# Kernel optimization log

Measured on AMD Instinct MI355X. Metric: run time of the kernel, lower is better.

## Reference

```python
import jax, jax.numpy as jnp
import numpy as np

N = 30000   # nodes
E = 480000  # directed edges (avg degree 16)
CIN = 64    # c_in
CH = 64     # c_hidden

_PARAM_NAMES = ["Wl1","bl1","Wr1","br1","We1","att1","bo1",
                "Wlm","blm","Wrm","brm","Wem","attm","bom",
                "Wl8","bl8","Wr8","br8","We8","att8","bo8"]
_PARAM_SHAPES = [(CIN,CH),(CH,),(CIN,CH),(CH,),(1,CH),(CH,),(CH,),
                 (6,CH,CH),(6,CH),(6,CH,CH),(6,CH),(6,1,CH),(6,CH),(6,CH),
                 (CH,1),(1,),(CH,1),(1,),(1,1),(1,),(1,)]

def setup_inputs() -> dict:
    key = jax.random.key(0)
    ks = jax.random.split(key, 4 + len(_PARAM_NAMES))
    inp = {
        "features": jax.random.normal(ks[0], (N, CIN), dtype=jnp.float32),
        "edge_src": jax.random.randint(ks[1], (E,), 0, N),
        "edge_dst": jax.random.randint(ks[2], (E,), 0, N),
        "edge_weight": jax.random.uniform(ks[3], (E,), dtype=jnp.float32),
    }
    for i, (name, shape) in enumerate(zip(_PARAM_NAMES, _PARAM_SHAPES)):
        inp[name] = jax.random.normal(ks[4 + i], shape, dtype=jnp.float32) * 0.05
    return inp

def _gatv2_layer(x, src, dst, attr, Wl, bl, Wr, br, We, att, bo):
    # PyG GATv2Conv, heads=1, negative_slope=0.2; (src,dst,attr) already include self-loops.
    n = x.shape[0]
    xl = x @ Wl + bl                                  # [N, C] source-side transform (lin_l)
    xr = x @ Wr + br                                  # [N, C] target-side transform (lin_r)
    e = xl[src] + xr[dst] + attr[:, None] * We[0]     # [Ea, C] per-edge pre-activation
    logit = jax.nn.leaky_relu(e, 0.2) @ att           # [Ea]
    m = jax.ops.segment_max(logit, dst, num_segments=n)
    z = jnp.exp(logit - m[dst])                       # stable softmax over each node's in-edges
    s = jax.ops.segment_sum(z, dst, num_segments=n)
    alpha = z / s[dst]                                # [Ea]
    return jax.ops.segment_sum(alpha[:, None] * xl[src], dst, num_segments=n) + bo

def reference(features, edge_src, edge_dst, edge_weight,
              Wl1, bl1, Wr1, br1, We1, att1, bo1,
              Wlm, blm, Wrm, brm, Wem, attm, bom,
              Wl8, bl8, Wr8, br8, We8, att8, bo8):
    n = features.shape[0]
    # add_self_loops=True with fill_value='mean': self-loop attr = mean of incoming edge attrs
    cnt = jax.ops.segment_sum(jnp.ones_like(edge_weight), edge_dst, num_segments=n)
    loop_attr = jax.ops.segment_sum(edge_weight, edge_dst, num_segments=n) / jnp.maximum(cnt, 1.0)
    loops = jnp.arange(n)
    src = jnp.concatenate([edge_src, loops])
    dst = jnp.concatenate([edge_dst, loops])
    attr = jnp.concatenate([edge_weight, loop_attr])
    x = _gatv2_layer(features, src, dst, attr, Wl1, bl1, Wr1, br1, We1, att1, bo1)
    for i in range(6):  # conv2..conv7, structurally identical hidden layers
        x = _gatv2_layer(x, src, dst, attr, Wlm[i], blm[i], Wrm[i], brm[i], Wem[i], attm[i], bom[i])
    x = _gatv2_layer(x, src, dst, attr, Wl8, bl8, Wr8, br8, We8, att8, bo8)  # [N, 1]
    return jnp.mean(x, axis=-2)  # mean pool over nodes -> [1]
```

## Files before the change

kernel.cpp:

```cpp
#include <hip/hip_runtime.h>
#include <math.h>

#define CH 64

__device__ __forceinline__ void multi_reduce8(const float lv[8], float L[8], int lane) {
  bool b5 = (lane & 32) != 0;
  float r1[4];
#pragma unroll
  for (int j = 0; j < 4; ++j) {
    float keep = b5 ? lv[j + 4] : lv[j];
    float send = b5 ? lv[j] : lv[j + 4];
    r1[j] = keep + __shfl_xor(send, 32, 64);
  }
  bool b4 = (lane & 16) != 0;
  float r2[2];
#pragma unroll
  for (int j = 0; j < 2; ++j) {
    float keep = b4 ? r1[j + 2] : r1[j];
    float send = b4 ? r1[j] : r1[j + 2];
    r2[j] = keep + __shfl_xor(send, 16, 64);
  }
  bool b3 = (lane & 8) != 0;
  float keep = b3 ? r2[1] : r2[0];
  float send = b3 ? r2[0] : r2[1];
  float v = keep + __shfl_xor(send, 8, 64);
  v += __shfl_xor(v, 4, 64);
  v += __shfl_xor(v, 2, 64);
  v += __shfl_xor(v, 1, 64);
#pragma unroll
  for (int j = 0; j < 8; ++j) L[j] = __shfl(v, j * 8, 64);
}


#define WSUM_SCALE 33554432.0f
#define WSUM_MASK 0xFFFFFFFFFFULL

__global__ void k_count(const int* __restrict__ dst, const float* __restrict__ w, int E,
                        unsigned long long* __restrict__ agg, int* __restrict__ rank) {
  int i = blockIdx.x * blockDim.x + threadIdx.x;
  if (i < E) {
    int d = dst[i];
    unsigned long long pk =
        (1ULL << 40) | (unsigned long long)(w[i] * WSUM_SCALE);
    unsigned long long old = atomicAdd(&agg[d], pk);
    rank[i] = (int)(old >> 40);
  }
}

__global__ void k_alloc(const unsigned long long* __restrict__ agg,
                        float* __restrict__ loop_attr, int* __restrict__ deg,
                        int* __restrict__ row_beg, int* __restrict__ total, int n) {
  int i = blockIdx.x * blockDim.x + threadIdx.x;
  int lane = threadIdx.x & 63;
  int d = 0;
  if (i < n) {
    unsigned long long v = agg[i];
    int c = (int)(v >> 40);
    float ws = (float)(v & WSUM_MASK) * (1.0f / WSUM_SCALE);
    loop_attr[i] = ws / fmaxf((float)c, 1.0f);
    d = c + 1;
    deg[i] = d;
  }
  int x = d;
#pragma unroll
  for (int off = 1; off < 64; off <<= 1) {
    int t = __shfl_up(x, off, 64);
    if (lane >= off) x += t;
  }
  int base = 0;
  if (lane == 63) base = atomicAdd(total, x);
  base = __shfl(base, 63, 64);
  if (i < n) row_beg[i] = base + x - d;
}

__global__ void k_scatter(const int* __restrict__ src, const int* __restrict__ dst,
                          const float* __restrict__ w, const int* __restrict__ rank, int E,
                          const int* __restrict__ row_beg, int2* __restrict__ csr) {
  int i = blockIdx.x * blockDim.x + threadIdx.x;
  if (i < E) {
    int d = dst[i];
    csr[row_beg[d] + rank[i]] = make_int2(src[i], __float_as_int(w[i]));
  }
}

__global__ void k_selfloop(int n, const int* __restrict__ row_beg, const int* __restrict__ deg,
                           int2* __restrict__ csr, const float* __restrict__ loop_attr) {
  int v = blockIdx.x * blockDim.x + threadIdx.x;
  if (v < n) {
    csr[row_beg[v] + deg[v] - 1] = make_int2(v, __float_as_int(loop_attr[v]));
  }
}


__global__ void __launch_bounds__(256) k_transform(
    const float* __restrict__ x, const float* __restrict__ Wl, const float* __restrict__ bl,
    const float* __restrict__ Wr, const float* __restrict__ br,
    float* __restrict__ xl, float* __restrict__ xr, int n) {
  __shared__ float sW[2][CH * CH];
  for (int i = threadIdx.x; i < (CH * CH) / 4; i += blockDim.x) {
    ((float4*)sW[0])[i] = ((const float4*)Wl)[i];
    ((float4*)sW[1])[i] = ((const float4*)Wr)[i];
  }
  __syncthreads();
  int lane = threadIdx.x & 63;
  int wid = threadIdx.x >> 6;
  float blc = bl[lane], brc = br[lane];
  int wavesPerGrid = (gridDim.x * blockDim.x) >> 6;
  for (int row = blockIdx.x * (blockDim.x >> 6) + wid; row < n; row += wavesPerGrid) {
    float xv = x[(size_t)row * CH + lane];
    float accl = blc, accr = brc;
#pragma unroll
    for (int k = 0; k < CH; ++k) {
      float xk = __shfl(xv, k, 64);
      accl = fmaf(xk, sW[0][k * CH + lane], accl);
      accr = fmaf(xk, sW[1][k * CH + lane], accr);
    }
    xl[(size_t)row * CH + lane] = accl;
    xr[(size_t)row * CH + lane] = accr;
  }
}


__global__ void __launch_bounds__(256) k_aggregate(
    const float* __restrict__ xl, const float* __restrict__ xr,
    const int* __restrict__ row_beg, const int* __restrict__ deg,
    const int2* __restrict__ csr,
    const float* __restrict__ We, const float* __restrict__ att, const float* __restrict__ bo,
    float* __restrict__ out, int n) {
  int lane = threadIdx.x & 63;
  int v = (blockIdx.x * blockDim.x + threadIdx.x) >> 6;
  if (v >= n) return;
  float Wec = We[lane], attc = att[lane], boc = bo[lane];
  float xrc = xr[(size_t)v * CH + lane];
  int beg = row_beg[v], dv = deg[v];
  float m = -INFINITY, s = 0.f, acc = 0.f;
  for (int chunk = 0; chunk < dv; chunk += 64) {
    int nc = min(64, dv - chunk);
    int2 ed = (lane < nc) ? csr[beg + chunk + lane] : make_int2(0, 0);
    for (int e = 0; e < nc; e += 8) {
      float xv[8], lv[8], L[8];
#pragma unroll
      for (int j = 0; j < 8; ++j) {
        int sj = __shfl(ed.x, e + j, 64);
        xv[j] = xl[(size_t)sj * CH + lane];
      }
#pragma unroll
      for (int j = 0; j < 8; ++j) {
        float aj = __int_as_float(__shfl(ed.y, e + j, 64));
        float ee = fmaf(aj, Wec, xv[j] + xrc);
        lv[j] = (ee > 0.f ? ee : 0.2f * ee) * attc;
      }
      multi_reduce8(lv, L, lane);
#pragma unroll
      for (int j = 0; j < 8; ++j)
        if (e + j >= nc) L[j] = -INFINITY;
      float bm = fmaxf(fmaxf(fmaxf(L[0], L[1]), fmaxf(L[2], L[3])),
                       fmaxf(fmaxf(L[4], L[5]), fmaxf(L[6], L[7])));
      float mn = fmaxf(m, bm);
      float sc = __expf(m - mn);
      float psum = 0.f, pdot = 0.f;
#pragma unroll
      for (int j = 0; j < 8; ++j) {
        float p = __expf(L[j] - mn);
        psum += p;
        pdot = fmaf(p, xv[j], pdot);
      }
      s = fmaf(s, sc, psum);
      acc = fmaf(acc, sc, pdot);
      m = mn;
    }
  }
  out[(size_t)v * CH + lane] = acc / s + boc;
}

__global__ void __launch_bounds__(256) k_transform8(
    const float* __restrict__ x, const float* __restrict__ Wl, const float* __restrict__ bl,
    const float* __restrict__ Wr, const float* __restrict__ br,
    float* __restrict__ xl8, float* __restrict__ xr8, int n) {
  int lane = threadIdx.x & 63;
  int v = (blockIdx.x * blockDim.x + threadIdx.x) >> 6;
  if (v >= n) return;
  float xv = x[(size_t)v * CH + lane];
  float a = xv * Wl[lane];
  float b = xv * Wr[lane];
#pragma unroll
  for (int off = 32; off > 0; off >>= 1) {
    a += __shfl_xor(a, off, 64);
    b += __shfl_xor(b, off, 64);
  }
  if (lane == 0) {
    xl8[v] = a + bl[0];
    xr8[v] = b + br[0];
  }
}

__global__ void __launch_bounds__(256) k_agg8_mean(
    const float* __restrict__ xl8, const float* __restrict__ xr8,
    const int* __restrict__ row_beg, const int* __restrict__ deg,
    const int2* __restrict__ csr,
    const float* __restrict__ We, const float* __restrict__ att, const float* __restrict__ bo,
    float* __restrict__ out, int n) {
  int lane = threadIdx.x & 63;
  int wid = threadIdx.x >> 6;
  float We0 = We[0], att0 = att[0], bo0 = bo[0];
  float inv_n = 1.0f / (float)n;
  float local = 0.f;
  int nwaves = gridDim.x * 4;
  for (int v = blockIdx.x * 4 + wid; v < n; v += nwaves) {
    float xrc = xr8[v];
    int beg = row_beg[v], dv = deg[v];
    float m = -INFINITY, s = 0.f, acc = 0.f;
    for (int chunk = 0; chunk < dv; chunk += 64) {
      int idx = chunk + lane;
      bool valid = idx < dv;
      int2 ed = valid ? csr[beg + idx] : make_int2(0, 0);
      float xlc = valid ? xl8[ed.x] : 0.f;
      float ee = fmaf(__int_as_float(ed.y), We0, xlc + xrc);
      float logit = valid ? (ee > 0.f ? ee : 0.2f * ee) * att0 : -INFINITY;
      float bm = logit;
#pragma unroll
      for (int off = 32; off > 0; off >>= 1) bm = fmaxf(bm, __shfl_xor(bm, off, 64));
      float mn = fmaxf(m, bm);
      float p = __expf(logit - mn);
      float pd = p * xlc;
#pragma unroll
      for (int off = 32; off > 0; off >>= 1) {
        p += __shfl_xor(p, off, 64);
        pd += __shfl_xor(pd, off, 64);
      }
      float sc = __expf(m - mn);
      s = fmaf(s, sc, p);
      acc = fmaf(acc, sc, pd);
      m = mn;
    }
    local += (acc / s + bo0) * inv_n;
  }
  __shared__ float sw[4];
  if (lane == 0) sw[wid] = local;
  __syncthreads();
  if (threadIdx.x == 0) atomicAdd(out, sw[0] + sw[1] + sw[2] + sw[3]);
}


extern "C" void kernel_launch(void* const* d_in, const int* in_sizes, int n_in,
                              void* d_out, int out_size, void* d_ws, size_t ws_size,
                              hipStream_t stream) {
  const float* features = (const float*)d_in[0];
  const int* edge_src = (const int*)d_in[1];
  const int* edge_dst = (const int*)d_in[2];
  const float* edge_w = (const float*)d_in[3];
  const int N = in_sizes[0] / CH;
  const int E = in_sizes[1];

  char* p = (char*)d_ws;
  auto take = [&](size_t bytes) {
    char* r = p;
    p += (bytes + 255) & ~(size_t)255;
    return r;
  };
  float* xA = (float*)take((size_t)N * CH * 4);
  float* xB = (float*)take((size_t)N * CH * 4);
  float* xl = (float*)take((size_t)N * CH * 4);
  float* xr = (float*)take((size_t)N * CH * 4);
  int2* csr = (int2*)take((size_t)(E + N) * 8);
  char* zero_region = take((size_t)N * 8 + 256);
  unsigned long long* agg = (unsigned long long*)zero_region;
  int* total = (int*)(zero_region + (size_t)N * 8);
  int* rank = (int*)take((size_t)E * 4);
  float* loop_attr = (float*)take((size_t)N * 4);
  int* deg = (int*)take((size_t)N * 4);
  int* row_beg = (int*)take((size_t)N * 4);
  float* xl8 = (float*)take((size_t)N * 4);
  float* xr8 = (float*)take((size_t)N * 4);

  hipMemsetAsync(zero_region, 0, (size_t)N * 8 + 256, stream);
  hipMemsetAsync(d_out, 0, sizeof(float), stream);

  const int tb = 256;
  k_count<<<(E + tb - 1) / tb, tb, 0, stream>>>(edge_dst, edge_w, E, agg, rank);
  k_alloc<<<(N + tb - 1) / tb, tb, 0, stream>>>(agg, loop_attr, deg, row_beg, total, N);
  k_scatter<<<(E + tb - 1) / tb, tb, 0, stream>>>(edge_src, edge_dst, edge_w, rank, E,
                                                  row_beg, csr);
  k_selfloop<<<(N + tb - 1) / tb, tb, 0, stream>>>(N, row_beg, deg, csr, loop_attr);

  const float* Wl1 = (const float*)d_in[4];
  const float* bl1 = (const float*)d_in[5];
  const float* Wr1 = (const float*)d_in[6];
  const float* br1 = (const float*)d_in[7];
  const float* We1 = (const float*)d_in[8];
  const float* att1 = (const float*)d_in[9];
  const float* bo1 = (const float*)d_in[10];
  const float* Wlm = (const float*)d_in[11];
  const float* blm = (const float*)d_in[12];
  const float* Wrm = (const float*)d_in[13];
  const float* brm = (const float*)d_in[14];
  const float* Wem = (const float*)d_in[15];
  const float* attm = (const float*)d_in[16];
  const float* bom = (const float*)d_in[17];

  const int agg_grid = ((size_t)N * 64 + tb - 1) / tb;
  const float* x_cur = features;
  float* x_nxt = xA;
  for (int layer = 0; layer < 7; ++layer) {
    const float *Wl, *bl, *Wr, *br, *We, *att, *bo;
    if (layer == 0) {
      Wl = Wl1; bl = bl1; Wr = Wr1; br = br1; We = We1; att = att1; bo = bo1;
    } else {
      int i = layer - 1;
      Wl = Wlm + (size_t)i * CH * CH;
      bl = blm + (size_t)i * CH;
      Wr = Wrm + (size_t)i * CH * CH;
      br = brm + (size_t)i * CH;
      We = Wem + (size_t)i * CH;
      att = attm + (size_t)i * CH;
      bo = bom + (size_t)i * CH;
    }
    k_transform<<<256, 256, 0, stream>>>(x_cur, Wl, bl, Wr, br, xl, xr, N);
    k_aggregate<<<agg_grid, tb, 0, stream>>>(xl, xr, row_beg, deg, csr, We, att, bo, x_nxt, N);
    x_cur = x_nxt;
    x_nxt = (x_nxt == xA) ? xB : xA;
  }
  k_transform8<<<agg_grid, tb, 0, stream>>>(
      x_cur, (const float*)d_in[18], (const float*)d_in[19], (const float*)d_in[20],
      (const float*)d_in[21], xl8, xr8, N);
  k_agg8_mean<<<1024, 256, 0, stream>>>(xl8, xr8, row_beg, deg, csr, (const float*)d_in[22],
                                        (const float*)d_in[23], (const float*)d_in[24],
                                        (float*)d_out, N);
}
```

Measured before the change: 667.4 us.

## Double-buffer neighbor gathers, fuse layer-8 transform into aggregate, widen transform grid

```diff
diff --git a/kernel.cpp b/kernel.cpp
--- a/kernel.cpp
+++ b/kernel.cpp
@@ -31,6 +31,75 @@
   for (int j = 0; j < 8; ++j) L[j] = __shfl(v, j * 8, 64);
 }
 
+struct AggState {
+  float m, s, acc;
+};
+
+__device__ __forceinline__ void agg_batch8(const float xv[8], const int2& ed, int e, int nc,
+                                           float Wec, float attc, float xrc, int lane,
+                                           AggState& st) {
+  float lv[8], L[8];
+#pragma unroll
+  for (int j = 0; j < 8; ++j) {
+    float aj = __int_as_float(__shfl(ed.y, e + j, 64));
+    float ee = fmaf(aj, Wec, xv[j] + xrc);
+    lv[j] = (ee > 0.f ? ee : 0.2f * ee) * attc;
+  }
+  multi_reduce8(lv, L, lane);
+#pragma unroll
+  for (int j = 0; j < 8; ++j)
+    if (e + j >= nc) L[j] = -INFINITY;
+  float bm = fmaxf(fmaxf(fmaxf(L[0], L[1]), fmaxf(L[2], L[3])),
+                   fmaxf(fmaxf(L[4], L[5]), fmaxf(L[6], L[7])));
+  float mn = fmaxf(st.m, bm);
+  float sc = __expf(st.m - mn);
+  float psum = 0.f, pdot = 0.f;
+#pragma unroll
+  for (int j = 0; j < 8; ++j) {
+    float p = __expf(L[j] - mn);
+    psum += p;
+    pdot = fmaf(p, xv[j], pdot);
+  }
+  st.s = fmaf(st.s, sc, psum);
+  st.acc = fmaf(st.acc, sc, pdot);
+  st.m = mn;
+}
+
+#define LOAD8(dst, ebase)                                          \
+  {                                                                \
+    _Pragma("unroll") for (int j = 0; j < 8; ++j) {                \
+      int sj = __shfl(ed.x, (ebase) + j, 64);                      \
+      dst[j] = xl[(size_t)sj * CH + lane];                         \
+    }                                                              \
+  }
+
+__device__ __forceinline__ AggState agg_node(const float* __restrict__ xl,
+                                             const int2* __restrict__ csr, int beg, int dv,
+                                             float Wec, float attc, float xrc, int lane) {
+  AggState st;
+  st.m = -INFINITY;
+  st.s = 0.f;
+  st.acc = 0.f;
+  for (int chunk = 0; chunk < dv; chunk += 64) {
+    int nc = min(64, dv - chunk);
+    int2 ed = (lane < nc) ? csr[beg + chunk + lane] : make_int2(0, 0);
+    float xva[8], xvb[8];
+    LOAD8(xva, 0);
+    int e = 0;
+    for (;;) {
+      if (e + 8 < nc) LOAD8(xvb, e + 8);
+      agg_batch8(xva, ed, e, nc, Wec, attc, xrc, lane, st);
+      e += 8;
+      if (e >= nc) break;
+      if (e + 8 < nc) LOAD8(xva, e + 8);
+      agg_batch8(xvb, ed, e, nc, Wec, attc, xrc, lane, st);
+      e += 8;
+      if (e >= nc) break;
+    }
+  }
+  return st;
+}
+
 
 #define WSUM_SCALE 33554432.0f
 #define WSUM_MASK 0xFFFFFFFFFFULL
@@ -40,8 +109,7 @@
   int i = blockIdx.x * blockDim.x + threadIdx.x;
   if (i < E) {
     int d = dst[i];
-    unsigned long long pk =
-        (1ULL << 40) | (unsigned long long)(w[i] * WSUM_SCALE);
+    unsigned long long pk = (1ULL << 40) | (unsigned long long)(w[i] * WSUM_SCALE);
     unsigned long long old = atomicAdd(&agg[d], pk);
     rank[i] = (int)(old >> 40);
   }
@@ -132,65 +200,35 @@
   if (v >= n) return;
   float Wec = We[lane], attc = att[lane], boc = bo[lane];
   float xrc = xr[(size_t)v * CH + lane];
-  int beg = row_beg[v], dv = deg[v];
-  float m = -INFINITY, s = 0.f, acc = 0.f;
-  for (int chunk = 0; chunk < dv; chunk += 64) {
-    int nc = min(64, dv - chunk);
-    int2 ed = (lane < nc) ? csr[beg + chunk + lane] : make_int2(0, 0);
-    for (int e = 0; e < nc; e += 8) {
-      float xv[8], lv[8], L[8];
-#pragma unroll
-      for (int j = 0; j < 8; ++j) {
-        int sj = __shfl(ed.x, e + j, 64);
-        xv[j] = xl[(size_t)sj * CH + lane];
-      }
-#pragma unroll
-      for (int j = 0; j < 8; ++j) {
-        float aj = __int_as_float(__shfl(ed.y, e + j, 64));
-        float ee = fmaf(aj, Wec, xv[j] + xrc);
-        lv[j] = (ee > 0.f ? ee : 0.2f * ee) * attc;
-      }
-      multi_reduce8(lv, L, lane);
-#pragma unroll
-      for (int j = 0; j < 8; ++j)
-        if (e + j >= nc) L[j] = -INFINITY;
-      float bm = fmaxf(fmaxf(fmaxf(L[0], L[1]), fmaxf(L[2], L[3])),
-                       fmaxf(fmaxf(L[4], L[5]), fmaxf(L[6], L[7])));
-      float mn = fmaxf(m, bm);
-      float sc = __expf(m - mn);
-      float psum = 0.f, pdot = 0.f;
-#pragma unroll
-      for (int j = 0; j < 8; ++j) {
-        float p = __expf(L[j] - mn);
-        psum += p;
-        pdot = fmaf(p, xv[j], pdot);
-      }
-      s = fmaf(s, sc, psum);
-      acc = fmaf(acc, sc, pdot);
-      m = mn;
-    }
-  }
-  out[(size_t)v * CH + lane] = acc / s + boc;
-}
-
-__global__ void __launch_bounds__(256) k_transform8(
-    const float* __restrict__ x, const float* __restrict__ Wl, const float* __restrict__ bl,
-    const float* __restrict__ Wr, const float* __restrict__ br,
+  AggState st = agg_node(xl, csr, row_beg[v], deg[v], Wec, attc, xrc, lane);
+  out[(size_t)v * CH + lane] = st.acc / st.s + boc;
+}
+
+__global__ void __launch_bounds__(256) k_aggregate_t8(
+    const float* __restrict__ xl, const float* __restrict__ xr,
+    const int* __restrict__ row_beg, const int* __restrict__ deg,
+    const int2* __restrict__ csr,
+    const float* __restrict__ We, const float* __restrict__ att, const float* __restrict__ bo,
+    const float* __restrict__ Wl8, const float* __restrict__ bl8,
+    const float* __restrict__ Wr8, const float* __restrict__ br8,
     float* __restrict__ xl8, float* __restrict__ xr8, int n) {
   int lane = threadIdx.x & 63;
   int v = (blockIdx.x * blockDim.x + threadIdx.x) >> 6;
   if (v >= n) return;
-  float xv = x[(size_t)v * CH + lane];
-  float a = xv * Wl[lane];
-  float b = xv * Wr[lane];
+  float Wec = We[lane], attc = att[lane], boc = bo[lane];
+  float xrc = xr[(size_t)v * CH + lane];
+  AggState st = agg_node(xl, csr, row_beg[v], deg[v], Wec, attc, xrc, lane);
+  float orow = st.acc / st.s + boc;
+  float a = orow * Wl8[lane];
+  float b = orow * Wr8[lane];
 #pragma unroll
   for (int off = 32; off > 0; off >>= 1) {
     a += __shfl_xor(a, off, 64);
     b += __shfl_xor(b, off, 64);
   }
   if (lane == 0) {
-    xl8[v] = a + bl[0];
-    xr8[v] = b + br[0];
+    xl8[v] = a + bl8[0];
+    xr8[v] = b + br8[0];
   }
 }
 
@@ -315,14 +353,18 @@
       att = attm + (size_t)i * CH;
       bo = bom + (size_t)i * CH;
     }
-    k_transform<<<256, 256, 0, stream>>>(x_cur, Wl, bl, Wr, br, xl, xr, N);
-    k_aggregate<<<agg_grid, tb, 0, stream>>>(xl, xr, row_beg, deg, csr, We, att, bo, x_nxt, N);
-    x_cur = x_nxt;
-    x_nxt = (x_nxt == xA) ? xB : xA;
-  }
-  k_transform8<<<agg_grid, tb, 0, stream>>>(
-      x_cur, (const float*)d_in[18], (const float*)d_in[19], (const float*)d_in[20],
-      (const float*)d_in[21], xl8, xr8, N);
+    k_transform<<<1024, 256, 0, stream>>>(x_cur, Wl, bl, Wr, br, xl, xr, N);
+    if (layer < 6) {
+      k_aggregate<<<agg_grid, tb, 0, stream>>>(xl, xr, row_beg, deg, csr, We, att, bo,
+                                               x_nxt, N);
+      x_cur = x_nxt;
+      x_nxt = (x_nxt == xA) ? xB : xA;
+    } else {
+      k_aggregate_t8<<<agg_grid, tb, 0, stream>>>(
+          xl, xr, row_beg, deg, csr, We, att, bo, (const float*)d_in[18],
+          (const float*)d_in[19], (const float*)d_in[20], (const float*)d_in[21], xl8, xr8, N);
+    }
+  }
   k_agg8_mean<<<1024, 256, 0, stream>>>(xl8, xr8, row_beg, deg, csr, (const float*)d_in[22],
                                         (const float*)d_in[23], (const float*)d_in[24],
                                         (float*)d_out, N);
```

New measurement: 629.3 us. 1.06x faster.
